# Optimization experiments

Hardware: AMD Instinct MI355X
Metric: run time of the kernel (lower is better)

The kernel has to match this reference:

```python
import jax, jax.numpy as jnp
import numpy as np

HEAD_SIZE = 64


def q_shift_multihead(x, ph, pw, head_dim=HEAD_SIZE, shift=1):
    # x: [B, T, C], T == ph*pw. Quarter-wise spatial shifts per head channel block.
    B, T, C = x.shape
    a = jnp.transpose(x, (0, 2, 1)).reshape(B, C // head_dim, head_dim, ph, pw)
    q = head_dim // 4
    out = jnp.zeros_like(a)
    out = out.at[:, :, 0:q, :, shift:].set(a[:, :, 0:q, :, :-shift])          # shift right in W
    out = out.at[:, :, q:2 * q, :, :-shift].set(a[:, :, q:2 * q, :, shift:])  # shift left in W
    out = out.at[:, :, 2 * q:3 * q, shift:, :].set(a[:, :, 2 * q:3 * q, :-shift, :])  # shift down in H
    out = out.at[:, :, 3 * q:, :-shift, :].set(a[:, :, 3 * q:, shift:, :])            # shift up in H
    return jnp.transpose(out.reshape(B, C, T), (0, 2, 1))


def wkv6(r, k, v, w, u):
    # RWKV-6 linear recurrence. r,k,v,w: [B,T,C]; u: [H, hs]. Decay applied as exp(-exp(w)).
    B, T, C = r.shape
    H, hs = C // HEAD_SIZE, HEAD_SIZE
    rh = jnp.transpose(r.reshape(B, T, H, hs), (1, 0, 2, 3))
    kh = jnp.transpose(k.reshape(B, T, H, hs), (1, 0, 2, 3))
    vh = jnp.transpose(v.reshape(B, T, H, hs), (1, 0, 2, 3))
    wh = jnp.exp(-jnp.exp(jnp.transpose(w.reshape(B, T, H, hs), (1, 0, 2, 3))))

    def step(S, inp):  # S: [B,H,hs(key j),hs(val i)]
        rt, kt, vt, wt = inp
        kv = kt[..., :, None] * vt[..., None, :]                # [B,H,hs,hs]
        y = jnp.einsum('bhj,bhji->bhi', rt, S + u[None, :, :, None] * kv)
        return wt[..., None] * S + kv, y

    S0 = jnp.zeros((B, H, hs, hs), r.dtype)
    _, ys = jax.lax.scan(step, S0, (rh, kh, vh, wh))
    return jnp.transpose(ys, (1, 0, 2, 3)).reshape(B, T, C)


def group_norm(x, weight, bias, n_groups, eps=1e-5):
    # x: [N, C]
    N, C = x.shape
    g = x.reshape(N, n_groups, C // n_groups)
    mu = g.mean(-1, keepdims=True)
    var = ((g - mu) ** 2).mean(-1, keepdims=True)
    g = (g - mu) / jnp.sqrt(var + eps)
    return g.reshape(N, C) * weight + bias


def setup_inputs() -> dict:
    key = jax.random.key(0)
    B, ph, pw, C = 8, 32, 32, 768
    T = ph * pw
    n_layer, layer_id = 12, 6
    H = C // HEAD_SIZE
    ks = jax.random.split(key, 10)
    x = jax.random.normal(ks[0], (B, T, C), jnp.float32)
    W_r = 0.02 * jax.random.normal(ks[1], (C, C), jnp.float32)
    W_k = 0.02 * jax.random.normal(ks[2], (C, C), jnp.float32)
    W_v = 0.02 * jax.random.normal(ks[3], (C, C), jnp.float32)
    W_g = 0.02 * jax.random.normal(ks[4], (C, C), jnp.float32)
    W_o = 0.02 * jax.random.normal(ks[5], (C, C), jnp.float32)
    r01 = layer_id / (n_layer - 1)
    r10 = 1.0 - layer_id / n_layer
    ddd = np.arange(C, dtype=np.float64) / C
    maa_x = jnp.asarray(1.0 - ddd ** r10, jnp.float32).reshape(1, 1, C)
    maa_w = maa_x
    maa_k = maa_x
    maa_v = jnp.asarray(1.0 - (ddd ** r10 + 0.3 * r01), jnp.float32).reshape(1, 1, C)
    maa_r = jnp.asarray(1.0 - ddd ** (0.5 * r10), jnp.float32).reshape(1, 1, C)
    maa_g = maa_r
    maa_w1 = jax.random.uniform(ks[6], (C, 32 * 5), jnp.float32, -1e-4, 1e-4)
    maa_w2 = jax.random.uniform(ks[7], (5, 32, C), jnp.float32, -1e-4, 1e-4)
    n = np.arange(C, dtype=np.float64)
    time_decay = jnp.asarray(-6 + 5 * (n / (C - 1)) ** (0.7 + 1.3 * r01), jnp.float32).reshape(1, 1, C)
    dec_w1 = jax.random.uniform(ks[8], (C, 64), jnp.float32, -1e-4, 1e-4)
    dec_w2 = jax.random.uniform(ks[9], (64, C), jnp.float32, -1e-4, 1e-4)
    zig = ((n + 1) % 3 - 1) * 0.1
    faaaa = jnp.asarray(r01 * (1 - n / (C - 1)) + zig, jnp.float32).reshape(H, HEAD_SIZE)
    ln_w = jnp.ones((C,), jnp.float32)
    ln_b = jnp.zeros((C,), jnp.float32)
    return dict(x=x, W_r=W_r, W_k=W_k, W_v=W_v, W_g=W_g, W_o=W_o,
                maa_x=maa_x, maa_w=maa_w, maa_k=maa_k, maa_v=maa_v, maa_r=maa_r, maa_g=maa_g,
                maa_w1=maa_w1, maa_w2=maa_w2, time_decay=time_decay,
                dec_w1=dec_w1, dec_w2=dec_w2, faaaa=faaaa, ln_w=ln_w, ln_b=ln_b,
                patch_h=ph, patch_w=pw)


def reference(x, W_r, W_k, W_v, W_g, W_o, maa_x, maa_w, maa_k, maa_v, maa_r, maa_g,
              maa_w1, maa_w2, time_decay, dec_w1, dec_w2, faaaa, ln_w, ln_b,
              patch_h, patch_w):
    B, T, C = x.shape
    xx = q_shift_multihead(x, patch_h, patch_w) - x
    xxx = x + xx * maa_x
    t = jnp.tanh(xxx @ maa_w1).reshape(B, T, 5, 32)
    m = jnp.einsum('btfr,frc->fbtc', t, maa_w2)  # [5,B,T,C]
    mw, mk, mv, mr, mg = m[0], m[1], m[2], m[3], m[4]
    xw = x + xx * (maa_w + mw)
    xk = x + xx * (maa_k + mk)
    xv = x + xx * (maa_v + mv)
    xr = x + xx * (maa_r + mr)
    xg = x + xx * (maa_g + mg)
    r = xr @ W_r.T
    k = xk @ W_k.T
    v = xv @ W_v.T
    g = jax.nn.relu(xg @ W_g.T)
    ww = jnp.tanh(xw @ dec_w1) @ dec_w2
    w = time_decay + ww
    y = wkv6(r, k, v, w, faaaa)
    y = group_norm(y.reshape(B * T, C), ln_w, ln_b, C // HEAD_SIZE).reshape(B, T, C)
    return (y * g) @ W_o.T
```

## Files before the change

kernel.cpp:

```cpp
#include <hip/hip_runtime.h>
#include <math.h>


#define EPI_NONE 0
#define EPI_TANH 1
#define EPI_RELU 2
#define EPI_BIAS 3

typedef float f32x4 __attribute__((ext_vector_type(4)));
typedef __bf16 bf16x8 __attribute__((ext_vector_type(8)));

__device__ __forceinline__ ushort f2bf(float x) {
  unsigned u = __float_as_uint(x);
  return (ushort)((u + 0x7fffu + ((u >> 16) & 1u)) >> 16);
}

#define GLDS16(gp, lp)                                                   \
  __builtin_amdgcn_global_load_lds(                                      \
      (const __attribute__((address_space(1))) void*)(gp),               \
      (__attribute__((address_space(3))) void*)(lp), 16, 0, 0)

__global__ __launch_bounds__(256) void k_prep(
    const float* __restrict__ x, const float* __restrict__ maa_x,
    ushort* __restrict__ xxx_bf,
    const float* __restrict__ w1, const float* __restrict__ w2,
    const float* __restrict__ dw1, const float* __restrict__ dw2,
    ushort* __restrict__ maa1T, ushort* __restrict__ w2T,
    ushort* __restrict__ w1dT, ushort* __restrict__ w2dT,
    int B, int T, int C, int ph, int pw) {
  long bx = blockIdx.x;
  const long QBLK = 24576;
  if (bx < QBLK) {
    long idx = bx * 256 + threadIdx.x;
    int c = (int)(idx % C);
    long bt = idx / C;
    int t = (int)(bt % T);
    int quarter = (c & 63) >> 4;
    int hh = t / pw;
    int ww = t - hh * pw;
    long rowbase = (bt - t) * C;
    float sval = 0.f;
    int st = -1;
    if (quarter == 0)      { if (ww >= 1)      st = t - 1;  }
    else if (quarter == 1) { if (ww < pw - 1)  st = t + 1;  }
    else if (quarter == 2) { if (hh >= 1)      st = t - pw; }
    else                   { if (hh < ph - 1)  st = t + pw; }
    if (st >= 0) sval = x[rowbase + (long)st * C + c];
    float xval = x[idx];
    float d = sval - xval;
    xxx_bf[idx] = f2bf(xval + d * maa_x[c]);
    return;
  }
  int idx = (int)(bx - QBLK) * 256 + threadIdx.x;
  if (idx < 196608) {
    int n = idx / 768, k = idx - n * 768;
    maa1T[idx] = f2bf(n < 160 ? w1[(size_t)k * 160 + n] : 0.f);
  } else if (idx < 196608 + 122880) {
    int j = idx - 196608;
    int c = j / 160, kk = j - c * 160;
    w2T[j] = f2bf(w2[(size_t)kk * 768 + c]);
  } else if (idx < 196608 + 122880 + 98304) {
    int j = idx - (196608 + 122880);
    int n = j / 768, k = j - n * 768;
    w1dT[j] = f2bf(n < 64 ? dw1[(size_t)k * 64 + n] : 0.f);
  } else {
    int j = idx - (196608 + 122880 + 98304);
    int n = j >> 6, k = j & 63;
    w2dT[j] = f2bf(dw2[(size_t)k * 768 + n]);
  }
}

__global__ __launch_bounds__(256) void k_mix5m(
    const ushort* __restrict__ t5b, const ushort* __restrict__ w2T,
    const float* __restrict__ x,
    const float* __restrict__ maa_w, const float* __restrict__ maa_k,
    const float* __restrict__ maa_v, const float* __restrict__ maa_r,
    const float* __restrict__ maa_g,
    ushort* __restrict__ xw, ushort* __restrict__ xk, ushort* __restrict__ xvb,
    ushort* __restrict__ xr, ushort* __restrict__ xg,
    int C, int T, int ph, int pw) {
  int tid = threadIdx.x;
  int lane = tid & 63, wid = tid >> 6;
  int m0 = blockIdx.y * 64, n0 = blockIdx.x * 128;
  int lm = lane & 15, lk = (lane >> 4) * 8;
  int rq = (lane >> 4) * 4;
  const ushort* ap = t5b + (size_t)(m0 + wid * 16 + lm) * 160 + lk;

  int stq[4][4];
#pragma unroll
  for (int q = 0; q < 4; q++) {
    int mr = m0 + wid * 16 + rq + q;
    int t = mr % T;
    int hh = t / pw, ww = t - hh * pw;
    stq[q][0] = (ww >= 1)      ? mr - 1  : -1;
    stq[q][1] = (ww < pw - 1)  ? mr + 1  : -1;
    stq[q][2] = (hh >= 1)      ? mr - pw : -1;
    stq[q][3] = (hh < ph - 1)  ? mr + pw : -1;
  }

  float xh[8][4], dh[8][4];
#pragma unroll
  for (int j = 0; j < 8; j++)
#pragma unroll
    for (int q = 0; q < 4; q++) {
      int mr = m0 + wid * 16 + rq + q;
      int col = n0 + j * 16 + lm;
      float xv = x[(size_t)mr * C + col];
      int sr = stq[q][j & 3];
      float sv = (sr >= 0) ? x[(size_t)sr * C + col] : 0.f;
      xh[j][q] = xv;
      dh[j][q] = sv - xv;
    }

#pragma unroll
  for (int f = 0; f < 5; f++) {
    bf16x8 af = *(const bf16x8*)(ap + f * 32);
    f32x4 acc[8];
#pragma unroll
    for (int j = 0; j < 8; j++) {
      bf16x8 bfj = *(const bf16x8*)(w2T +
          (size_t)(n0 + j * 16 + lm) * 160 + f * 32 + lk);
      acc[j] = __builtin_amdgcn_mfma_f32_16x16x32_bf16(
          af, bfj, (f32x4){0.f, 0.f, 0.f, 0.f}, 0, 0, 0);
    }
    const float* maa_f = (f == 0) ? maa_w : (f == 1) ? maa_k
                        : (f == 2) ? maa_v : (f == 3) ? maa_r : maa_g;
    ushort* dst = (f == 0) ? xw : (f == 1) ? xk
                 : (f == 2) ? xvb : (f == 3) ? xr : xg;
#pragma unroll
    for (int j = 0; j < 8; j++) {
      float mf = maa_f[n0 + j * 16 + lm];
#pragma unroll
      for (int q = 0; q < 4; q++) {
        size_t off = (size_t)(m0 + wid * 16 + rq + q) * C + (n0 + j * 16 + lm);
        dst[off] = f2bf(xh[j][q] + dh[j][q] * (mf + acc[j][q]));
      }
    }
  }
}

__global__ __launch_bounds__(256) void k_cvt5(
    const float* __restrict__ s0, const float* __restrict__ s1,
    const float* __restrict__ s2, const float* __restrict__ s3,
    const float* __restrict__ s4,
    ushort* __restrict__ d0, ushort* __restrict__ d1,
    ushort* __restrict__ d2, ushort* __restrict__ d3,
    ushort* __restrict__ d4, int n) {
  const float* s;
  ushort* d;
  switch (blockIdx.y) {
    case 0: s = s0; d = d0; break;
    case 1: s = s1; d = d1; break;
    case 2: s = s2; d = d2; break;
    case 3: s = s3; d = d3; break;
    default: s = s4; d = d4; break;
  }
  int i = (blockIdx.x * 256 + threadIdx.x) * 4;
  if (i >= n) return;
  float4 v = *(const float4*)(s + i);
  ushort4 o;
  o.x = f2bf(v.x); o.y = f2bf(v.y); o.z = f2bf(v.z); o.w = f2bf(v.w);
  *(ushort4*)(d + i) = o;
}

template <int EPI, bool NMASK, bool OBF16>
__global__ __launch_bounds__(256) void k_gemm_bf(
    const ushort* __restrict__ A, const ushort* __restrict__ W,
    const float* __restrict__ bias, void* __restrict__ Cm,
    int M, int N, int K) {
  __shared__ ushort Al[128 * 64];
  __shared__ ushort Bl[128 * 64];
  int nwg = gridDim.x * gridDim.y;
  int bid = blockIdx.y * gridDim.x + blockIdx.x;
  int swz = (nwg & 7) == 0 ? ((bid & 7) * (nwg >> 3) + (bid >> 3)) : bid;
  int bx = swz % gridDim.x, by = swz / gridDim.x;
  int m0 = by * 128, n0 = bx * 128;
  int tid = threadIdx.x;
  int lane = tid & 63, wave = tid >> 6;
  int wm = (wave >> 1) * 64, wn = (wave & 1) * 64;
  int lm = lane & 15, g = lane >> 4;
  f32x4 acc[4][4];
#pragma unroll
  for (int i = 0; i < 4; i++)
#pragma unroll
    for (int j = 0; j < 4; j++) acc[i][j] = (f32x4){0.f, 0.f, 0.f, 0.f};

  for (int k0 = 0; k0 < K; k0 += 64) {
#pragma unroll
    for (int i = 0; i < 4; i++) {
      int cid = tid + i * 256;
      int row = cid >> 3, p = cid & 7;
      int cq = p ^ (row & 7);
      GLDS16(A + (size_t)(m0 + row) * K + k0 + cq * 8, Al + cid * 8);
      GLDS16(W + (size_t)(n0 + row) * K + k0 + cq * 8, Bl + cid * 8);
    }
    __syncthreads();
#pragma unroll
    for (int s = 0; s < 2; s++) {
      bf16x8 af[4], bf[4];
#pragma unroll
      for (int i = 0; i < 4; i++) {
        int r = wm + i * 16 + lm;
        af[i] = *(const bf16x8*)&Al[r * 64 + (((s * 4 + g) ^ (r & 7)) * 8)];
        int rb = wn + i * 16 + lm;
        bf[i] = *(const bf16x8*)&Bl[rb * 64 + (((s * 4 + g) ^ (rb & 7)) * 8)];
      }
#pragma unroll
      for (int i = 0; i < 4; i++)
#pragma unroll
        for (int j = 0; j < 4; j++)
          acc[i][j] = __builtin_amdgcn_mfma_f32_16x16x32_bf16(
              af[i], bf[j], acc[i][j], 0, 0, 0);
    }
    __syncthreads();
  }
  int rq = (lane >> 4) * 4;
#pragma unroll
  for (int i = 0; i < 4; i++) {
#pragma unroll
    for (int j = 0; j < 4; j++) {
      int gn = n0 + wn + j * 16 + lm;
      if (NMASK && gn >= N) continue;
      float bv = (EPI == EPI_BIAS) ? bias[gn] : 0.f;
#pragma unroll
      for (int q = 0; q < 4; q++) {
        int gm = m0 + wm + i * 16 + rq + q;
        float val = acc[i][j][q];
        if (EPI == EPI_BIAS) val += bv;
        if (EPI == EPI_RELU) val = fmaxf(val, 0.f);
        if (EPI == EPI_TANH) val = tanhf(val);
        if (OBF16) ((ushort*)Cm)[(size_t)gm * N + gn] = f2bf(val);
        else       ((float*)Cm)[(size_t)gm * N + gn] = val;
      }
    }
  }
}

__global__ __launch_bounds__(256) void k_proj4(
    const ushort* __restrict__ A0, const ushort* __restrict__ A1,
    const ushort* __restrict__ A2, const ushort* __restrict__ A3,
    const ushort* __restrict__ W0, const ushort* __restrict__ W1,
    const ushort* __restrict__ W2, const ushort* __restrict__ W3,
    float* __restrict__ C0, float* __restrict__ C1,
    float* __restrict__ C2, float* __restrict__ C3,
    int M, int N, int K) {
  int nwg = gridDim.x;
  int bid = blockIdx.x;
  int swz = (bid & 7) * (nwg >> 3) + (bid >> 3);
  int nxt = N / 128;
  int per_z = (M / 128) * nxt;
  int z = swz / per_z;
  int rem = swz - z * per_z;
  int my = rem / nxt, nx = rem - my * nxt;
  const ushort* A = (z == 0) ? A0 : (z == 1) ? A1 : (z == 2) ? A2 : A3;
  const ushort* W = (z == 0) ? W0 : (z == 1) ? W1 : (z == 2) ? W2 : W3;
  float* Cm       = (z == 0) ? C0 : (z == 1) ? C1 : (z == 2) ? C2 : C3;
  __shared__ ushort Al[128 * 64];
  __shared__ ushort Bl[128 * 64];
  int tid = threadIdx.x;
  int m0 = my * 128, n0 = nx * 128;
  int lane = tid & 63, wave = tid >> 6;
  int wm = (wave >> 1) * 64, wn = (wave & 1) * 64;
  int lm = lane & 15, g = lane >> 4;
  f32x4 acc[4][4];
#pragma unroll
  for (int i = 0; i < 4; i++)
#pragma unroll
    for (int j = 0; j < 4; j++) acc[i][j] = (f32x4){0.f, 0.f, 0.f, 0.f};

  for (int k0 = 0; k0 < K; k0 += 64) {
#pragma unroll
    for (int i = 0; i < 4; i++) {
      int cid = tid + i * 256;
      int row = cid >> 3, p = cid & 7;
      int cq = p ^ (row & 7);
      GLDS16(A + (size_t)(m0 + row) * K + k0 + cq * 8, Al + cid * 8);
      GLDS16(W + (size_t)(n0 + row) * K + k0 + cq * 8, Bl + cid * 8);
    }
    __syncthreads();
#pragma unroll
    for (int s = 0; s < 2; s++) {
      bf16x8 af[4], bf[4];
#pragma unroll
      for (int i = 0; i < 4; i++) {
        int r = wm + i * 16 + lm;
        af[i] = *(const bf16x8*)&Al[r * 64 + (((s * 4 + g) ^ (r & 7)) * 8)];
        int rb = wn + i * 16 + lm;
        bf[i] = *(const bf16x8*)&Bl[rb * 64 + (((s * 4 + g) ^ (rb & 7)) * 8)];
      }
#pragma unroll
      for (int i = 0; i < 4; i++)
#pragma unroll
        for (int j = 0; j < 4; j++)
          acc[i][j] = __builtin_amdgcn_mfma_f32_16x16x32_bf16(
              af[i], bf[j], acc[i][j], 0, 0, 0);
    }
    __syncthreads();
  }
  bool relu = (z == 3);
  int rq = (lane >> 4) * 4;
#pragma unroll
  for (int i = 0; i < 4; i++) {
#pragma unroll
    for (int j = 0; j < 4; j++) {
      int gn = n0 + wn + j * 16 + lm;
#pragma unroll
      for (int q = 0; q < 4; q++) {
        int gm = m0 + wm + i * 16 + rq + q;
        float val = acc[i][j][q];
        if (relu) val = fmaxf(val, 0.f);
        Cm[(size_t)gm * N + gn] = val;
      }
    }
  }
}

__global__ __launch_bounds__(256) void k_decay(
    const ushort* __restrict__ xw, const ushort* __restrict__ w1dT,
    const ushort* __restrict__ w2dT, const float* __restrict__ time_dec,
    float* __restrict__ wout, int M, int C) {
  __shared__ ushort Al[128 * 64];
  __shared__ ushort Bl[128 * 64];
  int nwg = gridDim.x;
  int bid = blockIdx.x;
  int swz = (bid & 7) * (nwg >> 3) + (bid >> 3);
  int nxt = C / 128;
  int my = swz / nxt, nx = swz - my * nxt;
  int tid = threadIdx.x;
  int m0 = my * 128, n0 = nx * 128;
  int lane = tid & 63, wave = tid >> 6;
  int wm = (wave >> 1) * 64, wn = (wave & 1) * 64;
  int lm = lane & 15, g = lane >> 4;
  int rq = g * 4;
  f32x4 acc[4][4];
#pragma unroll
  for (int i = 0; i < 4; i++)
#pragma unroll
    for (int j = 0; j < 4; j++) acc[i][j] = (f32x4){0.f, 0.f, 0.f, 0.f};

  for (int k0 = 0; k0 < 768; k0 += 64) {
#pragma unroll
    for (int i = 0; i < 4; i++) {
      int cid = tid + i * 256;
      int row = cid >> 3, p = cid & 7;
      int cq = p ^ (row & 7);
      GLDS16(xw + (size_t)(m0 + row) * 768 + k0 + cq * 8, Al + cid * 8);
      GLDS16(w1dT + (size_t)row * 768 + k0 + cq * 8, Bl + cid * 8);
    }
    __syncthreads();
#pragma unroll
    for (int s = 0; s < 2; s++) {
      bf16x8 af[4], bf[4];
#pragma unroll
      for (int i = 0; i < 4; i++) {
        int r = wm + i * 16 + lm;
        af[i] = *(const bf16x8*)&Al[r * 64 + (((s * 4 + g) ^ (r & 7)) * 8)];
        int rb = wn + i * 16 + lm;
        bf[i] = *(const bf16x8*)&Bl[rb * 64 + (((s * 4 + g) ^ (rb & 7)) * 8)];
      }
#pragma unroll
      for (int i = 0; i < 4; i++)
#pragma unroll
        for (int j = 0; j < 4; j++)
          acc[i][j] = __builtin_amdgcn_mfma_f32_16x16x32_bf16(
              af[i], bf[j], acc[i][j], 0, 0, 0);
    }
    __syncthreads();
  }

#pragma unroll
  for (int i = 0; i < 4; i++) {
    int cid = tid + i * 256;
    int row = cid >> 3, p = cid & 7;
    int cq = p ^ (row & 7);
    GLDS16(w2dT + (size_t)(n0 + row) * 64 + cq * 8, Bl + cid * 8);
  }
  if (wn == 0) {
#pragma unroll
    for (int i = 0; i < 4; i++)
#pragma unroll
      for (int j = 0; j < 4; j++)
#pragma unroll
        for (int q = 0; q < 4; q++) {
          int row = wm + i * 16 + rq + q;
          int col = j * 16 + lm;
          int ch = (col >> 3) ^ (row & 7);
          Al[row * 64 + ch * 8 + (col & 7)] = f2bf(tanhf(acc[i][j][q]));
        }
  }
  __syncthreads();

  f32x4 acc2[4][4];
#pragma unroll
  for (int i = 0; i < 4; i++)
#pragma unroll
    for (int j = 0; j < 4; j++) acc2[i][j] = (f32x4){0.f, 0.f, 0.f, 0.f};
#pragma unroll
  for (int s = 0; s < 2; s++) {
    bf16x8 af[4], bf[4];
#pragma unroll
    for (int i = 0; i < 4; i++) {
      int r = wm + i * 16 + lm;
      af[i] = *(const bf16x8*)&Al[r * 64 + (((s * 4 + g) ^ (r & 7)) * 8)];
      int rb = wn + i * 16 + lm;
      bf[i] = *(const bf16x8*)&Bl[rb * 64 + (((s * 4 + g) ^ (rb & 7)) * 8)];
    }
#pragma unroll
    for (int i = 0; i < 4; i++)
#pragma unroll
      for (int j = 0; j < 4; j++)
        acc2[i][j] = __builtin_amdgcn_mfma_f32_16x16x32_bf16(
            af[i], bf[j], acc2[i][j], 0, 0, 0);
  }
#pragma unroll
  for (int i = 0; i < 4; i++) {
#pragma unroll
    for (int j = 0; j < 4; j++) {
      int gn = n0 + wn + j * 16 + lm;
      float bv = time_dec[gn];
#pragma unroll
      for (int q = 0; q < 4; q++) {
        int gm = m0 + wm + i * 16 + rq + q;
        wout[(size_t)gm * C + gn] = bv + acc2[i][j][q];
      }
    }
  }
}

__global__ __launch_bounds__(256) void k_wkv_prekv(
    const float* __restrict__ k, const float* __restrict__ w,
    const float* __restrict__ v,
    float* __restrict__ aL, float* __restrict__ kvb,
    int B, int T, int C, int H, int L) {
  __shared__ float Ks[64 * 64];
  __shared__ float Vs[64 * 64];
  __shared__ float gsum[4 * 64];
  int nch = T / L;
  int blk = blockIdx.x;
  int bh = blk / nch, c = blk - bh * nch;
  int b = bh / H, h = bh - b * H;
  int tid = threadIdx.x;
  int gsel = tid >> 6;
  int j = tid & 63;
  long cbase = ((long)b * T + (long)c * L) * C + h * 64;

#pragma unroll
  for (int i = 0; i < 4; i++) {
    int chunk = gsel * 4 + i;
    int row = chunk * 4 + (j >> 4);
    int cq = j & 15;
    GLDS16(v + cbase + (long)row * C + cq * 4, Vs + chunk * 256);
  }

  int tau0 = gsel * 16;
  float ev[16];
#pragma unroll
  for (int i = 0; i < 16; i++)
    ev[i] = expf(w[cbase + (long)(tau0 + i) * C + j]);
  float pre[16];
  float run = 0.f;
#pragma unroll
  for (int i = 0; i < 16; i++) { pre[i] = run; run += ev[i]; }
  gsum[gsel * 64 + j] = run;
  __syncthreads();
  float off0 = (gsel > 0 ? gsum[j] : 0.f) +
               (gsel > 1 ? gsum[64 + j] : 0.f) +
               (gsel > 2 ? gsum[128 + j] : 0.f);
  if (gsel == 3)
    aL[((long)bh * nch + c) * 64 + j] = expf(-(off0 + run));

#pragma unroll
  for (int i = 0; i < 16; i++) {
    float kv = k[cbase + (long)(tau0 + i) * C + j];
    Ks[(tau0 + i) * 64 + j] = kv * expf(off0 + pre[i] + ev[i]);
  }
  __syncthreads();

  int lane = tid & 63, jg = tid >> 6;
  float acc[16];
#pragma unroll
  for (int q = 0; q < 16; q++) acc[q] = 0.f;
  for (int s = 0; s < 64; s++) {
    float vi = Vs[s * 64 + lane];
#pragma unroll
    for (int q4 = 0; q4 < 4; q4++) {
      float4 kk = *(const float4*)(Ks + s * 64 + jg * 16 + q4 * 4);
      acc[q4 * 4 + 0] = fmaf(kk.x, vi, acc[q4 * 4 + 0]);
      acc[q4 * 4 + 1] = fmaf(kk.y, vi, acc[q4 * 4 + 1]);
      acc[q4 * 4 + 2] = fmaf(kk.z, vi, acc[q4 * 4 + 2]);
      acc[q4 * 4 + 3] = fmaf(kk.w, vi, acc[q4 * 4 + 3]);
    }
  }
  float* out = kvb + ((long)bh * nch + c) * 4096;
#pragma unroll
  for (int q = 0; q < 16; q++) out[(jg * 16 + q) * 64 + lane] = acc[q];
}

__global__ __launch_bounds__(256) void k_wkv_scan(
    const float* __restrict__ kvb, const float* __restrict__ aL,
    float* __restrict__ Scb, int nch) {
  int bh = blockIdx.x >> 4;
  int e = ((blockIdx.x & 15) << 8) + threadIdx.x;
  float S = 0.f;
  for (int c = 0; c < nch; c++) {
    long cb = ((long)bh * nch + c) * 4096 + e;
    Scb[cb] = S;
    S = aL[((long)bh * nch + c) * 64 + (e >> 6)] * (S + kvb[cb]);
  }
}

__global__ __launch_bounds__(256, 3) void k_wkv_intra(
    const float* __restrict__ r, const float* __restrict__ k,
    const float* __restrict__ w, const float* __restrict__ u,
    const float* __restrict__ v, const float* __restrict__ Scb,
    const float* __restrict__ g,
    const float* __restrict__ ln_w, const float* __restrict__ ln_b,
    ushort* __restrict__ z, int B, int T, int C, int H, int L) {
  int nch = T / L;
  int blk = blockIdx.x;
  int bh = blk / nch, c = blk - bh * nch;
  int b = bh / H, h = bh - b * H;
  __shared__ float KtT[64 * 68];
  __shared__ float RtT[64 * 68];
  __shared__ float Pt[64 * 68];
  __shared__ float gsum[4 * 64];
  __shared__ float pdv[64];
  int tid = threadIdx.x;
  int lane = tid & 63, wid = tid >> 6;
  long cbase = ((long)b * T + (long)c * L) * C + h * 64;
  const float* scp = Scb + ((long)bh * nch + c) * 4096;

  {
    int gsel = wid;
    int j = lane;
    int tau0p = gsel * 16;
    float uj = u[h * 64 + j];
    float ev[16];
#pragma unroll
    for (int i = 0; i < 16; i++)
      ev[i] = expf(w[cbase + (long)(tau0p + i) * C + j]);
    float pre[16];
    float run = 0.f;
#pragma unroll
    for (int i = 0; i < 16; i++) { pre[i] = run; run += ev[i]; }
    gsum[gsel * 64 + j] = run;
    __syncthreads();
    float off0 = (gsel > 0 ? gsum[j] : 0.f) +
                 (gsel > 1 ? gsum[64 + j] : 0.f) +
                 (gsel > 2 ? gsum[128 + j] : 0.f);
#pragma unroll
    for (int i = 0; i < 16; i++) {
      int tau = tau0p + i;
      long offg = cbase + (long)tau * C + j;
      float rv = r[offg];
      float kv = k[offg];
      float ce = off0 + pre[i];
      RtT[j * 68 + tau] = rv * expf(-ce);
      KtT[j * 68 + tau] = kv * expf(ce + ev[i]);
      Pt[tau * 68 + j] = rv * uj * kv;
    }
  }
  __syncthreads();
  if (tid < 64) {
    float s0 = 0.f, s1 = 0.f, s2 = 0.f, s3 = 0.f;
#pragma unroll
    for (int q = 0; q < 16; q++) {
      float4 p4 = *(const float4*)(Pt + tid * 68 + q * 4);
      s0 += p4.x; s1 += p4.y; s2 += p4.z; s3 += p4.w;
    }
    pdv[tid] = (s0 + s1) + (s2 + s3);
  }
  __syncthreads();

  {
    int s0 = (tid >> 4) * 4;
    int tau0 = (tid & 15) * 4;
    float4 pd4 = *(const float4*)(pdv + tau0);
    float p00 = 0.f, p01 = 0.f, p02 = 0.f, p03 = 0.f;
    float p10 = 0.f, p11 = 0.f, p12 = 0.f, p13 = 0.f;
    float p20 = 0.f, p21 = 0.f, p22 = 0.f, p23 = 0.f;
    float p30 = 0.f, p31 = 0.f, p32 = 0.f, p33 = 0.f;
#pragma unroll 4
    for (int cc = 0; cc < 64; cc++) {
      float4 kq = *(const float4*)(KtT + cc * 68 + s0);
      float4 rq = *(const float4*)(RtT + cc * 68 + tau0);
      p00 = fmaf(kq.x, rq.x, p00); p01 = fmaf(kq.x, rq.y, p01);
      p02 = fmaf(kq.x, rq.z, p02); p03 = fmaf(kq.x, rq.w, p03);
      p10 = fmaf(kq.y, rq.x, p10); p11 = fmaf(kq.y, rq.y, p11);
      p12 = fmaf(kq.y, rq.z, p12); p13 = fmaf(kq.y, rq.w, p13);
      p20 = fmaf(kq.z, rq.x, p20); p21 = fmaf(kq.z, rq.y, p21);
      p22 = fmaf(kq.z, rq.z, p22); p23 = fmaf(kq.z, rq.w, p23);
      p30 = fmaf(kq.w, rq.x, p30); p31 = fmaf(kq.w, rq.y, p31);
      p32 = fmaf(kq.w, rq.z, p32); p33 = fmaf(kq.w, rq.w, p33);
    }
#define PMASK(PI0, PI1, PI2, PI3, I)                                       \
    {                                                                      \
      int s = s0 + (I);                                                    \
      float4 o;                                                            \
      o.x = (s < tau0 + 0) ? PI0 : (s == tau0 + 0 ? pd4.x : 0.f);          \
      o.y = (s < tau0 + 1) ? PI1 : (s == tau0 + 1 ? pd4.y : 0.f);          \
      o.z = (s < tau0 + 2) ? PI2 : (s == tau0 + 2 ? pd4.z : 0.f);          \
      o.w = (s < tau0 + 3) ? PI3 : (s == tau0 + 3 ? pd4.w : 0.f);          \
      *(float4*)(Pt + s * 68 + tau0) = o;                                  \
    }
    PMASK(p00, p01, p02, p03, 0)
    PMASK(p10, p11, p12, p13, 1)
    PMASK(p20, p21, p22, p23, 2)
    PMASK(p30, p31, p32, p33, 3)
#undef PMASK
  }
  __syncthreads();

  int row0 = wid * 16 + ((lane >> 4) << 2);
  int c0v = (lane & 15) * 4;
  float4 acc0 = {0.f, 0.f, 0.f, 0.f};
  float4 acc1 = {0.f, 0.f, 0.f, 0.f};
  float4 acc2 = {0.f, 0.f, 0.f, 0.f};
  float4 acc3 = {0.f, 0.f, 0.f, 0.f};
  const float* vp = v + cbase + c0v;
#define FMA2(A, P, V4, R, S4)                          \
  A.x = fmaf(P, V4.x, fmaf(R, S4.x, A.x));             \
  A.y = fmaf(P, V4.y, fmaf(R, S4.y, A.y));             \
  A.z = fmaf(P, V4.z, fmaf(R, S4.z, A.z));             \
  A.w = fmaf(P, V4.w, fmaf(R, S4.w, A.w));
#pragma unroll 4
  for (int j = 0; j < 64; j++) {
    float4 pp = *(const float4*)(Pt + j * 68 + row0);
    float4 rr = *(const float4*)(RtT + j * 68 + row0);
    float4 vv = *(const float4*)(vp + (long)j * C);
    float4 ssv = *(const float4*)(scp + j * 64 + c0v);
    FMA2(acc0, pp.x, vv, rr.x, ssv);
    FMA2(acc1, pp.y, vv, rr.y, ssv);
    FMA2(acc2, pp.z, vv, rr.z, ssv);
    FMA2(acc3, pp.w, vv, rr.w, ssv);
  }
#undef FMA2

  float4 lw4 = *(const float4*)(ln_w + h * 64 + c0v);
  float4 lb4 = *(const float4*)(ln_b + h * 64 + c0v);
#define GNROW(A, m)                                                        \
  {                                                                        \
    float s1 = (A.x + A.y) + (A.z + A.w);                                  \
    s1 += __shfl_xor(s1, 1, 64);                                           \
    s1 += __shfl_xor(s1, 2, 64);                                           \
    s1 += __shfl_xor(s1, 4, 64);                                           \
    s1 += __shfl_xor(s1, 8, 64);                                           \
    float mu = s1 * (1.f / 64.f);                                          \
    float4 dd;                                                             \
    dd.x = A.x - mu; dd.y = A.y - mu; dd.z = A.z - mu; dd.w = A.w - mu;    \
    float s2 = (dd.x * dd.x + dd.y * dd.y) + (dd.z * dd.z + dd.w * dd.w);  \
    s2 += __shfl_xor(s2, 1, 64);                                           \
    s2 += __shfl_xor(s2, 2, 64);                                           \
    s2 += __shfl_xor(s2, 4, 64);                                           \
    s2 += __shfl_xor(s2, 8, 64);                                           \
    float rstd = rsqrtf(s2 * (1.f / 64.f) + 1e-5f);                        \
    long off = cbase + (long)(row0 + m) * C + c0v;                         \
    float4 g4 = *(const float4*)(g + off);                                 \
    ushort4 ob;                                                            \
    ob.x = f2bf((dd.x * rstd * lw4.x + lb4.x) * g4.x);                     \
    ob.y = f2bf((dd.y * rstd * lw4.y + lb4.y) * g4.y);                     \
    ob.z = f2bf((dd.z * rstd * lw4.z + lb4.z) * g4.z);                     \
    ob.w = f2bf((dd.w * rstd * lw4.w + lb4.w) * g4.w);                     \
    *(ushort4*)(z + off) = ob;                                             \
  }
  GNROW(acc0, 0)
  GNROW(acc1, 1)
  GNROW(acc2, 2)
  GNROW(acc3, 3)
#undef GNROW
}

extern "C" void kernel_launch(void* const* d_in, const int* in_sizes, int n_in,
                              void* d_out, int out_size, void* d_ws, size_t ws_size,
                              hipStream_t stream) {
  const int B = 8, T = 1024, C = 768, H = 12, ph = 32, pw = 32;
  const int M = B * T;
  const int L = 64, NCH = T / L;

  const float* x        = (const float*)d_in[0];
  const float* W_r      = (const float*)d_in[1];
  const float* W_k      = (const float*)d_in[2];
  const float* W_v      = (const float*)d_in[3];
  const float* W_g      = (const float*)d_in[4];
  const float* W_o      = (const float*)d_in[5];
  const float* maa_x    = (const float*)d_in[6];
  const float* maa_w    = (const float*)d_in[7];
  const float* maa_k    = (const float*)d_in[8];
  const float* maa_v    = (const float*)d_in[9];
  const float* maa_r    = (const float*)d_in[10];
  const float* maa_g    = (const float*)d_in[11];
  const float* maa_w1   = (const float*)d_in[12];
  const float* maa_w2   = (const float*)d_in[13];
  const float* time_dec = (const float*)d_in[14];
  const float* dec_w1   = (const float*)d_in[15];
  const float* dec_w2   = (const float*)d_in[16];
  const float* faaaa    = (const float*)d_in[17];
  const float* ln_w     = (const float*)d_in[18];
  const float* ln_b     = (const float*)d_in[19];

  float* ws = (float*)d_ws;
  const size_t S = (size_t)M * C;
  float* F0 = ws + 0 * S;
  float* F1 = ws + 1 * S;
  float* F2 = ws + 2 * S;
  float* F3 = ws + 3 * S;
  float* F4 = ws + 4 * S;
  float* F5 = ws + 5 * S;
  float* F6 = ws + 6 * S;
  float* t5    = ws + 7 * S;
  float* t6    = t5 + (size_t)M * 160;
  float* aLb   = t6 + (size_t)M * 64;
  float* pdiag = aLb + (size_t)B * H * NCH * 64;
  float* dec_t = pdiag + (size_t)B * H * T;

  ushort* xxx_bf = (ushort*)F1;
  ushort* xw_bf = (ushort*)F2;
  ushort* xr_bf = (ushort*)F5;
  ushort* xk_bf = xr_bf + S;
  ushort* xv_bf = (ushort*)F6;
  ushort* xg_bf = xv_bf + S;
  float*  kvb   = F6;
  ushort* z_bf  = (ushort*)F6;
  float*  wdec  = F5;
  float*  Scb   = F2;
  ushort* t5b   = (ushort*)t5;
  ushort* w2T   = (ushort*)dec_t;
  const int WSZ = C * C;
  ushort* wr_bf = (ushort*)t5;
  ushort* wk_bf = wr_bf + WSZ;
  ushort* wv_bf = wk_bf + WSZ;
  ushort* wg_bf = wv_bf + WSZ;
  ushort* wo_bf = (ushort*)t6;
  ushort* maa1T = wo_bf + WSZ;
  ushort* w1dT  = maa1T + 256 * 768;
  ushort* w2dT  = w1dT + 128 * 768;

  {
    k_prep<<<24576 + 1824, 256, 0, stream>>>(
        x, maa_x, xxx_bf, maa_w1, maa_w2, dec_w1, dec_w2,
        maa1T, w2T, w1dT, w2dT, B, T, C, ph, pw);
  }
  {
    dim3 grid(2, M / 128);
    k_gemm_bf<EPI_TANH, true, true><<<grid, 256, 0, stream>>>(
        xxx_bf, maa1T, nullptr, t5b, M, 160, C);
  }
  {
    dim3 grid(C / 128, M / 64);
    k_mix5m<<<grid, 256, 0, stream>>>(t5b, w2T, x, maa_w, maa_k, maa_v,
                                      maa_r, maa_g, xw_bf, xk_bf, xv_bf, xr_bf,
                                      xg_bf, C, T, ph, pw);
  }
  {
    dim3 grid((WSZ / 4 + 255) / 256, 5);
    k_cvt5<<<grid, 256, 0, stream>>>(W_r, W_k, W_v, W_g, W_o,
                                     wr_bf, wk_bf, wv_bf, wg_bf, wo_bf, WSZ);
  }
  {
    k_proj4<<<(C / 128) * (M / 128) * 4, 256, 0, stream>>>(
        xr_bf, xk_bf, xv_bf, xg_bf, wr_bf, wk_bf, wv_bf, wg_bf,
        F0, F1, F3, F4, M, C, C);
  }
  {
    k_decay<<<(M / 128) * (C / 128), 256, 0, stream>>>(
        xw_bf, w1dT, w2dT, time_dec, wdec, M, C);
  }
  k_wkv_prekv<<<B * H * NCH, 256, 0, stream>>>(
      F1, wdec, F3, aLb, kvb, B, T, C, H, L);
  k_wkv_scan<<<B * H * 16, 256, 0, stream>>>(kvb, aLb, Scb, NCH);
  k_wkv_intra<<<B * H * NCH, 256, 0, stream>>>(
      F0, F1, wdec, faaaa, F3, Scb, F4, ln_w, ln_b, z_bf, B, T, C, H, L);
  {
    dim3 grid(C / 128, M / 128);
    k_gemm_bf<EPI_NONE, false, false><<<grid, 256, 0, stream>>>(
        z_bf, wo_bf, nullptr, (float*)d_out, M, C, C);
  }
}
```

Measured before the change: 361.4 us.

## Compute decay LoRA first stage once per row block; drop Pt LDS buffer in wkv_intra

k_decay now launches one block per 128-row tile and loops over all six 128-column output tiles, so the first-stage xw@dec_w1 product and tanh are computed once per row tile instead of six times. This cuts that redundant GEMM work but leaves only M/128 blocks (64), which may underfill the GPU. In k_wkv_intra the diagonal u-term is now reduced with wave shuffles, and the P matrix reuses the KtT buffer instead of a separate Pt array. That frees LDS so launch bounds can be raised from 3 to 4 blocks per CU, at the cost of an extra barrier.

```diff
diff --git a/kernel.cpp b/kernel.cpp
--- a/kernel.cpp
+++ b/kernel.cpp
@@ -321,13 +321,8 @@
     float* __restrict__ wout, int M, int C) {
   __shared__ ushort Al[128 * 64];
   __shared__ ushort Bl[128 * 64];
-  int nwg = gridDim.x;
-  int bid = blockIdx.x;
-  int swz = (bid & 7) * (nwg >> 3) + (bid >> 3);
-  int nxt = C / 128;
-  int my = swz / nxt, nx = swz - my * nxt;
   int tid = threadIdx.x;
-  int m0 = my * 128, n0 = nx * 128;
+  int m0 = blockIdx.x * 128;
   int lane = tid & 63, wave = tid >> 6;
   int wm = (wave >> 1) * 64, wn = (wave & 1) * 64;
   int lm = lane & 15, g = lane >> 4;
@@ -368,13 +363,6 @@
     __syncthreads();
   }
 
-#pragma unroll
-  for (int i = 0; i < 4; i++) {
-    int cid = tid + i * 256;
-    int row = cid >> 3, p = cid & 7;
-    int cq = p ^ (row & 7);
-    GLDS16(w2dT + (size_t)(n0 + row) * 64 + cq * 8, Bl + cid * 8);
-  }
   if (wn == 0) {
 #pragma unroll
     for (int i = 0; i < 4; i++)
@@ -388,42 +376,53 @@
           Al[row * 64 + ch * 8 + (col & 7)] = f2bf(tanhf(acc[i][j][q]));
         }
   }
-  __syncthreads();
-
-  f32x4 acc2[4][4];
-#pragma unroll
-  for (int i = 0; i < 4; i++)
-#pragma unroll
-    for (int j = 0; j < 4; j++) acc2[i][j] = (f32x4){0.f, 0.f, 0.f, 0.f};
-#pragma unroll
-  for (int s = 0; s < 2; s++) {
-    bf16x8 af[4], bf[4];
+
+  for (int nx = 0; nx < 6; nx++) {
+    int n0 = nx * 128;
 #pragma unroll
     for (int i = 0; i < 4; i++) {
-      int r = wm + i * 16 + lm;
-      af[i] = *(const bf16x8*)&Al[r * 64 + (((s * 4 + g) ^ (r & 7)) * 8)];
-      int rb = wn + i * 16 + lm;
-      bf[i] = *(const bf16x8*)&Bl[rb * 64 + (((s * 4 + g) ^ (rb & 7)) * 8)];
-    }
+      int cid = tid + i * 256;
+      int row = cid >> 3, p = cid & 7;
+      int cq = p ^ (row & 7);
+      GLDS16(w2dT + (size_t)(n0 + row) * 64 + cq * 8, Bl + cid * 8);
+    }
+    __syncthreads();
+    f32x4 acc2[4][4];
 #pragma unroll
     for (int i = 0; i < 4; i++)
 #pragma unroll
-      for (int j = 0; j < 4; j++)
-        acc2[i][j] = __builtin_amdgcn_mfma_f32_16x16x32_bf16(
-            af[i], bf[j], acc2[i][j], 0, 0, 0);
-  }
-#pragma unroll
-  for (int i = 0; i < 4; i++) {
-#pragma unroll
-    for (int j = 0; j < 4; j++) {
-      int gn = n0 + wn + j * 16 + lm;
-      float bv = time_dec[gn];
-#pragma unroll
-      for (int q = 0; q < 4; q++) {
-        int gm = m0 + wm + i * 16 + rq + q;
-        wout[(size_t)gm * C + gn] = bv + acc2[i][j][q];
+      for (int j = 0; j < 4; j++) acc2[i][j] = (f32x4){0.f, 0.f, 0.f, 0.f};
+#pragma unroll
+    for (int s = 0; s < 2; s++) {
+      bf16x8 af[4], bf[4];
+#pragma unroll
+      for (int i = 0; i < 4; i++) {
+        int r = wm + i * 16 + lm;
+        af[i] = *(const bf16x8*)&Al[r * 64 + (((s * 4 + g) ^ (r & 7)) * 8)];
+        int rb = wn + i * 16 + lm;
+        bf[i] = *(const bf16x8*)&Bl[rb * 64 + (((s * 4 + g) ^ (rb & 7)) * 8)];
       }
-    }
+#pragma unroll
+      for (int i = 0; i < 4; i++)
+#pragma unroll
+        for (int j = 0; j < 4; j++)
+          acc2[i][j] = __builtin_amdgcn_mfma_f32_16x16x32_bf16(
+              af[i], bf[j], acc2[i][j], 0, 0, 0);
+    }
+#pragma unroll
+    for (int i = 0; i < 4; i++) {
+#pragma unroll
+      for (int j = 0; j < 4; j++) {
+        int gn = n0 + wn + j * 16 + lm;
+        float bv = time_dec[gn];
+#pragma unroll
+        for (int q = 0; q < 4; q++) {
+          int gm = m0 + wm + i * 16 + rq + q;
+          wout[(size_t)gm * C + gn] = bv + acc2[i][j][q];
+        }
+      }
+    }
+    __syncthreads();
   }
 }
 
@@ -509,7 +508,7 @@
   }
 }
 
-__global__ __launch_bounds__(256, 3) void k_wkv_intra(
+__global__ __launch_bounds__(256, 4) void k_wkv_intra(
     const float* __restrict__ r, const float* __restrict__ k,
     const float* __restrict__ w, const float* __restrict__ u,
     const float* __restrict__ v, const float* __restrict__ Scb,
@@ -522,7 +521,6 @@
   int b = bh / H, h = bh - b * H;
   __shared__ float KtT[64 * 68];
   __shared__ float RtT[64 * 68];
-  __shared__ float Pt[64 * 68];
   __shared__ float gsum[4 * 64];
   __shared__ float pdv[64];
   int tid = threadIdx.x;
@@ -557,24 +555,18 @@
       float ce = off0 + pre[i];
       RtT[j * 68 + tau] = rv * expf(-ce);
       KtT[j * 68 + tau] = kv * expf(ce + ev[i]);
-      Pt[tau * 68 + j] = rv * uj * kv;
+      float pd = rv * uj * kv;
+#pragma unroll
+      for (int o = 32; o >= 1; o >>= 1) pd += __shfl_xor(pd, o, 64);
+      if (lane == 0) pdv[tau] = pd;
     }
   }
   __syncthreads();
-  if (tid < 64) {
-    float s0 = 0.f, s1 = 0.f, s2 = 0.f, s3 = 0.f;
-#pragma unroll
-    for (int q = 0; q < 16; q++) {
-      float4 p4 = *(const float4*)(Pt + tid * 68 + q * 4);
-      s0 += p4.x; s1 += p4.y; s2 += p4.z; s3 += p4.w;
-    }
-    pdv[tid] = (s0 + s1) + (s2 + s3);
-  }
-  __syncthreads();
-
-  {
-    int s0 = (tid >> 4) * 4;
-    int tau0 = (tid & 15) * 4;
+
+  int s0 = (tid >> 4) * 4;
+  int tau0 = (tid & 15) * 4;
+  float4 o0, o1, o2, o3;
+  {
     float4 pd4 = *(const float4*)(pdv + tau0);
     float p00 = 0.f, p01 = 0.f, p02 = 0.f, p03 = 0.f;
     float p10 = 0.f, p11 = 0.f, p12 = 0.f, p13 = 0.f;
@@ -593,22 +585,25 @@
       p30 = fmaf(kq.w, rq.x, p30); p31 = fmaf(kq.w, rq.y, p31);
       p32 = fmaf(kq.w, rq.z, p32); p33 = fmaf(kq.w, rq.w, p33);
     }
-#define PMASK(PI0, PI1, PI2, PI3, I)                                       \
+#define PMASK(O, PI0, PI1, PI2, PI3, I)                                    \
     {                                                                      \
       int s = s0 + (I);                                                    \
-      float4 o;                                                            \
-      o.x = (s < tau0 + 0) ? PI0 : (s == tau0 + 0 ? pd4.x : 0.f);          \
-      o.y = (s < tau0 + 1) ? PI1 : (s == tau0 + 1 ? pd4.y : 0.f);          \
-      o.z = (s < tau0 + 2) ? PI2 : (s == tau0 + 2 ? pd4.z : 0.f);          \
-      o.w = (s < tau0 + 3) ? PI3 : (s == tau0 + 3 ? pd4.w : 0.f);          \
-      *(float4*)(Pt + s * 68 + tau0) = o;                                  \
-    }
-    PMASK(p00, p01, p02, p03, 0)
-    PMASK(p10, p11, p12, p13, 1)
-    PMASK(p20, p21, p22, p23, 2)
-    PMASK(p30, p31, p32, p33, 3)
+      O.x = (s < tau0 + 0) ? PI0 : (s == tau0 + 0 ? pd4.x : 0.f);          \
+      O.y = (s < tau0 + 1) ? PI1 : (s == tau0 + 1 ? pd4.y : 0.f);          \
+      O.z = (s < tau0 + 2) ? PI2 : (s == tau0 + 2 ? pd4.z : 0.f);          \
+      O.w = (s < tau0 + 3) ? PI3 : (s == tau0 + 3 ? pd4.w : 0.f);          \
+    }
+    PMASK(o0, p00, p01, p02, p03, 0)
+    PMASK(o1, p10, p11, p12, p13, 1)
+    PMASK(o2, p20, p21, p22, p23, 2)
+    PMASK(o3, p30, p31, p32, p33, 3)
 #undef PMASK
   }
+  __syncthreads();
+  *(float4*)(KtT + (s0 + 0) * 68 + tau0) = o0;
+  *(float4*)(KtT + (s0 + 1) * 68 + tau0) = o1;
+  *(float4*)(KtT + (s0 + 2) * 68 + tau0) = o2;
+  *(float4*)(KtT + (s0 + 3) * 68 + tau0) = o3;
   __syncthreads();
 
   int row0 = wid * 16 + ((lane >> 4) << 2);
@@ -625,7 +620,7 @@
   A.w = fmaf(P, V4.w, fmaf(R, S4.w, A.w));
 #pragma unroll 4
   for (int j = 0; j < 64; j++) {
-    float4 pp = *(const float4*)(Pt + j * 68 + row0);
+    float4 pp = *(const float4*)(KtT + j * 68 + row0);
     float4 rr = *(const float4*)(RtT + j * 68 + row0);
     float4 vv = *(const float4*)(vp + (long)j * C);
     float4 ssv = *(const float4*)(scp + j * 64 + c0v);
@@ -762,7 +757,7 @@
         F0, F1, F3, F4, M, C, C);
   }
   {
-    k_decay<<<(M / 128) * (C / 128), 256, 0, stream>>>(
+    k_decay<<<M / 128, 256, 0, stream>>>(
         xw_bf, w1dT, w2dT, time_dec, wdec, M, C);
   }
   k_wkv_prekv<<<B * H * NCH, 256, 0, stream>>>(
```

Measured after the change: 385.9 us. +6.8%, slower.
